# Kernel optimization log

Measured on AMD Instinct MI355X. Metric: run time of the kernel, lower is better.

Reference implementation:

```python
import jax, jax.numpy as jnp
import numpy as np

D_IN = 2048
D_OUT = 2048
H = 16
QK_ROPE = 64
QK_NOPE = 64
QK_HEAD = QK_NOPE + QK_ROPE  # 128
V_HEAD = 128
KV_RANK = 512
THETA = 10000.0
EPS = 1e-6


def rms_norm(x, w):
    var = jnp.mean(x * x, axis=-1, keepdims=True)
    return x * jax.lax.rsqrt(var + EPS) * w


def apply_rope(x, theta=THETA):
    # x: [B, S, H, D] with D even; interleaved-pair rotation (torchtune style)
    B, S, NH, D = x.shape
    half = D // 2
    freqs = 1.0 / (theta ** (jnp.arange(0, D, 2, dtype=jnp.float32) / D))  # [D/2]
    ang = jnp.arange(S, dtype=jnp.float32)[:, None] * freqs[None, :]       # [S, D/2]
    cos = jnp.cos(ang)[None, :, None, :]  # [1,S,1,D/2]
    sin = jnp.sin(ang)[None, :, None, :]
    xp = x.reshape(B, S, NH, half, 2)
    x1, x2 = xp[..., 0], xp[..., 1]
    out = jnp.stack([x1 * cos - x2 * sin, x2 * cos + x1 * sin], axis=-1)
    return out.reshape(B, S, NH, D).astype(x.dtype)


def setup_inputs() -> dict:
    key = jax.random.key(0)
    ks = jax.random.split(key, 6)
    B, S = 2, 2048
    s = lambda fan_in: 1.0 / np.sqrt(fan_in)
    x = jax.random.normal(ks[0], (B, S, D_IN), dtype=jnp.float32)
    w_query = jax.random.uniform(ks[1], (D_IN, H * QK_HEAD), jnp.float32, -s(D_IN), s(D_IN))
    wkv_a = jax.random.uniform(ks[2], (D_IN, KV_RANK + QK_ROPE), jnp.float32, -s(D_IN), s(D_IN))
    wkv_b = jax.random.uniform(ks[3], (KV_RANK, H * (QK_NOPE + V_HEAD)), jnp.float32, -s(KV_RANK), s(KV_RANK))
    kv_norm_w = jnp.ones((KV_RANK,), jnp.float32)
    out_proj_w = jax.random.uniform(ks[4], (H * V_HEAD, D_OUT), jnp.float32, -s(H * V_HEAD), s(H * V_HEAD))
    return {"x": x, "w_query": w_query, "wkv_a": wkv_a, "wkv_b": wkv_b,
            "kv_norm_w": kv_norm_w, "out_proj_w": out_proj_w}


def reference(x, w_query, wkv_a, wkv_b, kv_norm_w, out_proj_w):
    B, S, _ = x.shape
    scale = QK_HEAD ** -0.5
    # queries (no q-lora)
    q = (x @ w_query).reshape(B, S, H, QK_HEAD)
    # low-rank KV compression
    kv = x @ wkv_a                                    # [B,S,KV_RANK+QK_ROPE]
    kv_c, k_pe = kv[..., :KV_RANK], kv[..., KV_RANK:]
    kv_dec = (rms_norm(kv_c, kv_norm_w) @ wkv_b).reshape(B, S, H, QK_NOPE + V_HEAD)
    k_nope, v = kv_dec[..., :QK_NOPE], kv_dec[..., QK_NOPE:]
    k_pe = jnp.broadcast_to(k_pe[:, :, None, :], (B, S, H, QK_ROPE))
    q_nope, q_pe = q[..., :QK_NOPE], q[..., QK_NOPE:]
    q_pe = apply_rope(q_pe)
    k_pe = apply_rope(k_pe)
    queries = jnp.concatenate([q_nope, q_pe], axis=-1)   # [B,S,H,QK_HEAD]
    keys = jnp.concatenate([k_nope, k_pe], axis=-1)
    # attention
    scores = jnp.einsum('bqhd,bkhd->bhqk', queries, keys) * scale
    mask = jnp.triu(jnp.ones((S, S), dtype=bool), k=1)
    scores = jnp.where(mask[None, None], -jnp.inf, scores)
    attn = jax.nn.softmax(scores.astype(jnp.float32), axis=-1).astype(x.dtype)
    out = jnp.einsum('bhqk,bkhd->bqhd', attn, v).reshape(B, S, H * V_HEAD)
    return out @ out_proj_w
```

## Files before the change

kernel.cpp:

```cpp
#include <hip/hip_runtime.h>
#include <hip/hip_bf16.h>
#include <math.h>

#define BATCH   2
#define SEQ     2048
#define D_IN    2048
#define NHEAD   16
#define QK_ROPE 64
#define QK_NOPE 64
#define QK_HEAD 128
#define V_HEAD  128
#define KV_RANK 512
#define KV_W    640
#define NTOK    (BATCH*SEQ)
#define EPS_F   1e-6f

typedef unsigned short u16;
typedef short bf16x8 __attribute__((ext_vector_type(8)));
typedef float f32x4  __attribute__((ext_vector_type(4)));

__device__ __forceinline__ u16 f2bf(float f) {
    unsigned u = __float_as_uint(f);
    return (u16)((u + 0x7fffu + ((u >> 16) & 1u)) >> 16);
}
__device__ __forceinline__ float bf2f(u16 u) {
    return __uint_as_float(((unsigned)u) << 16);
}
__device__ __forceinline__ float exp2_hw(float x) {
    float r;
    asm volatile("v_exp_f32 %0, %1\n\ts_nop 0" : "=v"(r) : "v"(x));
    return r;
}
__device__ __forceinline__ void gload16(const void* g, void* l) {
    __builtin_amdgcn_global_load_lds((const __attribute__((address_space(1))) unsigned int*)g,
                                     (__attribute__((address_space(3))) unsigned int*)l, 16, 0, 0);
}

__global__ __launch_bounds__(256) void convert_bf16(const float* __restrict__ src,
                                                    u16* __restrict__ dst, int n4) {
    int gid = blockIdx.x * 256 + threadIdx.x;
    if (gid >= n4) return;
    float4 v = ((const float4*)src)[gid];
    unsigned lo = (unsigned)f2bf(v.x) | ((unsigned)f2bf(v.y) << 16);
    unsigned hi = (unsigned)f2bf(v.z) | ((unsigned)f2bf(v.w) << 16);
    ((uint2*)dst)[gid] = make_uint2(lo, hi);
}

__global__ __launch_bounds__(256) void transpose_bf16(const float* __restrict__ src,
                                                      u16* __restrict__ dst,
                                                      int N, int K) {
    __shared__ float tile[32][33];
    const int nb = blockIdx.x * 32, kb = blockIdx.y * 32;
    const int tx = threadIdx.x, ty = threadIdx.y;
#pragma unroll
    for (int i = 0; i < 4; ++i) {
        int k = kb + ty + 8 * i, n = nb + tx;
        tile[ty + 8 * i][tx] = (n < N) ? src[(size_t)k * N + n] : 0.f;
    }
    __syncthreads();
#pragma unroll
    for (int i = 0; i < 4; ++i) {
        int n = nb + ty + 8 * i, k = kb + tx;
        dst[(size_t)n * K + k] = f2bf(tile[tx][ty + 8 * i]);
    }
}

__global__ __launch_bounds__(256) void rope_table_kernel(float* __restrict__ tab) {
    int gid = blockIdx.x * 256 + threadIdx.x;
    int i = gid & 31, s = gid >> 5;
    float freq = __expf(-(float)(2 * i) / 64.0f * 9.210340371976184f);
    float ang = (float)s * freq;
    tab[2 * gid]     = cosf(ang);
    tab[2 * gid + 1] = sinf(ang);
}

template <int EPI>
__global__ __launch_bounds__(512, 1) void gemm256(const u16* __restrict__ A,
                                                  const u16* __restrict__ BT,
                                                  void* __restrict__ out0,
                                                  void* __restrict__ out1,
                                                  const float* __restrict__ tab,
                                                  int gx, int N, int K, float oscale) {
    __shared__ u16 lds[65536];
    const int tid = threadIdx.x;
    const int w = tid >> 6, l = tid & 63;
    const int lr = l & 15, lg = l >> 4;
    const int wr = w >> 2;
    const int wc = w & 3;
    const int nwg = gridDim.x, q8 = nwg >> 3;
    const int wg = (blockIdx.x & 7) * q8 + (blockIdx.x >> 3);
    const int row0 = (wg / gx) * 256, col0 = (wg % gx) * 256;
    const int NT = K >> 6;

    f32x4 acc[8][4];
#pragma unroll
    for (int m = 0; m < 8; ++m)
#pragma unroll
        for (int n = 0; n < 4; ++n) acc[m][n] = (f32x4){0.f, 0.f, 0.f, 0.f};

    auto stageA = [&](int bufi, int h, int kt) {
        u16* base = lds + bufi * 16384 + h * 8192;
        const u16* g = A + (size_t)(row0 + h * 128) * K + kt * 64;
#pragma unroll
        for (int i = 0; i < 2; ++i) {
            int L = (i * 512 + tid) * 16;
            int s = L ^ (((L >> 7) & 7) << 4);
            gload16(g + (size_t)(s >> 7) * K + ((s & 127) >> 1), base + (L >> 1));
        }
    };
    auto stageB = [&](int bufi, int h, int kt) {
        u16* base = lds + 32768 + bufi * 16384 + h * 8192;
        const u16* g = BT + (size_t)(col0 + h * 128) * K + kt * 64;
#pragma unroll
        for (int i = 0; i < 2; ++i) {
            int L = (i * 512 + tid) * 16;
            int s = L ^ (((L >> 7) & 7) << 4);
            gload16(g + (size_t)(s >> 7) * K + ((s & 127) >> 1), base + (L >> 1));
        }
    };

    stageB(0, 0, 0); stageB(0, 1, 0); stageA(0, 0, 0); stageA(0, 1, 0);

    const int bhalf = wc >> 1;
    const int brow0 = (wc & 1) * 64;

    for (int t = 0; t < NT; ++t) {
        const int buf = t & 1, nb = buf ^ 1;
        u16* Ab = lds + buf * 16384 + wr * 8192;
        u16* Bb = lds + 32768 + buf * 16384 + bhalf * 8192;

#pragma unroll
        for (int q = 0; q < 4; ++q) {
            const int mh = q >> 1, ks = q & 1;
            if (q == 0) {
                asm volatile("s_waitcnt vmcnt(2)" ::: "memory");
                __builtin_amdgcn_s_barrier();
                __builtin_amdgcn_sched_barrier(0);
            } else if (q == 2) {
                if (t + 1 < NT) asm volatile("s_waitcnt vmcnt(4)" ::: "memory");
                else            asm volatile("s_waitcnt vmcnt(0)" ::: "memory");
                __builtin_amdgcn_s_barrier();
                __builtin_amdgcn_sched_barrier(0);
            }
            bf16x8 af[4], bfg[4];
#pragma unroll
            for (int i = 0; i < 4; ++i) {
                int row = (mh * 4 + i) * 16 + lr;
                int byte = row * 128 + ks * 64 + lg * 16;
                af[i] = *(const bf16x8*)&Ab[(byte ^ ((row & 7) << 4)) >> 1];
            }
#pragma unroll
            for (int n = 0; n < 4; ++n) {
                int row = brow0 + n * 16 + lr;
                int byte = row * 128 + ks * 64 + lg * 16;
                bfg[n] = *(const bf16x8*)&Bb[(byte ^ ((row & 7) << 4)) >> 1];
            }
            if (t + 1 < NT) {
                if (q == 0)      stageB(nb, 0, t + 1);
                else if (q == 1) stageB(nb, 1, t + 1);
                else if (q == 2) stageA(nb, 0, t + 1);
                else             stageA(nb, 1, t + 1);
            }
            __builtin_amdgcn_s_barrier();
            asm volatile("s_waitcnt lgkmcnt(0)" ::: "memory");
            __builtin_amdgcn_sched_barrier(0);
            __builtin_amdgcn_s_setprio(1);
#pragma unroll
            for (int i = 0; i < 4; ++i)
#pragma unroll
                for (int n = 0; n < 4; ++n)
                    acc[mh * 4 + i][n] = __builtin_amdgcn_mfma_f32_16x16x32_bf16(
                        af[i], bfg[n], acc[mh * 4 + i][n], 0, 0, 0);
            __builtin_amdgcn_s_setprio(0);
        }
    }

    if (EPI == 0) {
        u16* qp = (u16*)out0;
        float* kvp = (float*)out1;
        const bool pe = (wc & 1);
#pragma unroll
        for (int m = 0; m < 8; ++m)
#pragma unroll
            for (int n = 0; n < 4; ++n) {
                int c = col0 + wc * 64 + n * 16 + lr;
#pragma unroll
                for (int j = 0; j < 4; ++j) {
                    int r = row0 + wr * 128 + m * 16 + 4 * lg + j;
                    float v = acc[m][n][j];
                    if (c < 2048) {
                        v *= oscale;
                        if (pe) {
                            int s = r & (SEQ - 1);
                            int ip = (16 * n + lr) >> 1;
                            float2 cs = ((const float2*)tab)[s * 32 + ip];
                            float part = __shfl_xor(v, 1);
                            v = (lr & 1) ? (v * cs.x + part * cs.y)
                                         : (v * cs.x - part * cs.y);
                        }
                        qp[(size_t)r * 2048 + c] = f2bf(v);
                    } else if (c < 2688) {
                        kvp[(size_t)r * KV_W + (c - 2048)] = v;
                    }
                }
            }
    } else {
        u16* Kall = (u16*)out0;
        u16* Vt   = (u16*)out1;
#pragma unroll
        for (int m = 0; m < 8; ++m) {
            int r0 = row0 + wr * 128 + m * 16 + 4 * lg;
            int b  = r0 >> 11;
            int s0 = r0 & (SEQ - 1);
#pragma unroll
            for (int n = 0; n < 4; ++n) {
                int c = col0 + wc * 64 + n * 16 + lr;
                int h = (unsigned)c / 192u;
                int cr = c - h * 192;
                int bh = b * NHEAD + h;
                if (cr < 64) {
#pragma unroll
                    for (int j = 0; j < 4; ++j) {
                        int s = s0 + j;
                        Kall[((size_t)bh * SEQ + s) * 128 + (cr ^ ((s & 7) << 3))] = f2bf(acc[m][n][j]);
                    }
                } else {
                    int d = cr - 64;
                    union { u16 u[4]; uint2 v; } pk;
#pragma unroll
                    for (int j = 0; j < 4; ++j) pk.u[j] = f2bf(acc[m][n][j]);
                    size_t base = ((size_t)bh * 128 + d) * SEQ + (s0 & ~63);
                    *(uint2*)&Vt[base + ((s0 & 63) ^ ((d & 7) << 3))] = pk.v;
                }
            }
        }
    }
}

__global__ __launch_bounds__(512, 1) void gemm_out(const u16* __restrict__ A,
                                                   const u16* __restrict__ BT,
                                                   float* __restrict__ C,
                                                   int N, int K) {
    __shared__ u16 lds[73728];
    const int tid = threadIdx.x;
    const int w = tid >> 6, l = tid & 63;
    const int lr = l & 15, lg = l >> 4;
    const int wr = w >> 1, wc = w & 1;
    const int nwg = gridDim.x, q8 = nwg >> 3;
    const int wg = (blockIdx.x & 7) * q8 + (blockIdx.x >> 3);
    const int gx = N >> 7;
    const int row0 = (wg / gx) * 256, col0 = (wg % gx) * 128;
    const int NT = K >> 6;

    f32x4 acc[4][4];
#pragma unroll
    for (int m = 0; m < 4; ++m)
#pragma unroll
        for (int n = 0; n < 4; ++n) acc[m][n] = (f32x4){0.f, 0.f, 0.f, 0.f};

    auto stageA = [&](int bufi, int h, int kt) {
        u16* base = lds + bufi * 16384 + h * 8192;
        const u16* g = A + (size_t)(row0 + h * 128) * K + kt * 64;
#pragma unroll
        for (int i = 0; i < 2; ++i) {
            int L = (i * 512 + tid) * 16;
            int s = L ^ (((L >> 7) & 7) << 4);
            gload16(g + (size_t)(s >> 7) * K + ((s & 127) >> 1), base + (L >> 1));
        }
    };
    auto stageB = [&](int bufi, int kt) {
        u16* base = lds + 49152 + bufi * 8192;
        const u16* g = BT + (size_t)col0 * K + kt * 64;
#pragma unroll
        for (int i = 0; i < 2; ++i) {
            int L = (i * 512 + tid) * 16;
            int s = L ^ (((L >> 7) & 7) << 4);
            gload16(g + (size_t)(s >> 7) * K + ((s & 127) >> 1), base + (L >> 1));
        }
    };

    stageA(0, 0, 0); stageA(0, 1, 0); stageB(0, 0);
    stageA(1, 0, 1); stageA(1, 1, 1); stageB(1, 1);

    const int ar0 = (wr & 1) * 64;

    for (int t = 0; t < NT; ++t) {
        const int buf = t % 3, nb2 = (t + 2) % 3;
        u16* Ab = lds + buf * 16384 + (wr >> 1) * 8192;
        u16* Bb = lds + 49152 + buf * 8192;
        if (t + 1 < NT) asm volatile("s_waitcnt vmcnt(6)" ::: "memory");
        else            asm volatile("s_waitcnt vmcnt(0)" ::: "memory");
        __builtin_amdgcn_s_barrier();
        __builtin_amdgcn_sched_barrier(0);

#pragma unroll
        for (int q = 0; q < 2; ++q) {
            bf16x8 af[4], bfg[4];
#pragma unroll
            for (int i = 0; i < 4; ++i) {
                int row = ar0 + i * 16 + lr;
                int byte = row * 128 + q * 64 + lg * 16;
                af[i] = *(const bf16x8*)&Ab[(byte ^ ((row & 7) << 4)) >> 1];
            }
#pragma unroll
            for (int n = 0; n < 4; ++n) {
                int row = wc * 64 + n * 16 + lr;
                int byte = row * 128 + q * 64 + lg * 16;
                bfg[n] = *(const bf16x8*)&Bb[(byte ^ ((row & 7) << 4)) >> 1];
            }
            if (t + 2 < NT) {
                if (q == 0) { stageA(nb2, 0, t + 2); stageA(nb2, 1, t + 2); }
                else        { stageB(nb2, t + 2); }
            }
            __builtin_amdgcn_s_barrier();
            asm volatile("s_waitcnt lgkmcnt(0)" ::: "memory");
            __builtin_amdgcn_sched_barrier(0);
            __builtin_amdgcn_s_setprio(1);
#pragma unroll
            for (int i = 0; i < 4; ++i)
#pragma unroll
                for (int n = 0; n < 4; ++n)
                    acc[i][n] = __builtin_amdgcn_mfma_f32_16x16x32_bf16(
                        af[i], bfg[n], acc[i][n], 0, 0, 0);
            __builtin_amdgcn_s_setprio(0);
        }
    }

#pragma unroll
    for (int m = 0; m < 4; ++m)
#pragma unroll
        for (int n = 0; n < 4; ++n) {
            int c = col0 + wc * 64 + n * 16 + lr;
#pragma unroll
            for (int j = 0; j < 4; ++j) {
                int r = row0 + wr * 64 + m * 16 + 4 * lg + j;
                C[(size_t)r * N + c] = acc[m][n][j];
            }
        }
}

__global__ __launch_bounds__(256) void rmsnorm_bf(const float* __restrict__ kv,
                                                  const float* __restrict__ w,
                                                  u16* __restrict__ c_norm) {
    __shared__ float red[256];
    const int row = blockIdx.x, t = threadIdx.x;
    const float* src = kv + (size_t)row * KV_W;
    float v0 = src[t], v1 = src[t + 256];
    red[t] = v0 * v0 + v1 * v1;
    __syncthreads();
    for (int s = 128; s > 0; s >>= 1) {
        if (t < s) red[t] += red[t + s];
        __syncthreads();
    }
    const float inv = rsqrtf(red[0] / (float)KV_RANK + EPS_F);
    u16* dst = c_norm + (size_t)row * KV_RANK;
    dst[t]       = f2bf(v0 * inv * w[t]);
    dst[t + 256] = f2bf(v1 * inv * w[t + 256]);
}

__global__ __launch_bounds__(256) void build_kpe(const float* __restrict__ kv,
                                                 const float* __restrict__ tab,
                                                 u16* __restrict__ K_all) {
    const int gid = blockIdx.x * 256 + threadIdx.x;
    const int dq = gid & 15;
    const int s = (gid >> 4) & (SEQ - 1);
    const int b = gid >> 15;
    const float* src = kv + (size_t)(b * SEQ + s) * KV_W + KV_RANK + 4 * dq;
    float4 v = *(const float4*)src;
    const int i0 = 2 * dq;
    float2 cs0 = ((const float2*)tab)[s * 32 + i0];
    float2 cs1 = ((const float2*)tab)[s * 32 + i0 + 1];
    union { u16 u[4]; uint2 w; } pk;
    pk.u[0] = f2bf(v.x * cs0.x - v.y * cs0.y);
    pk.u[1] = f2bf(v.y * cs0.x + v.x * cs0.y);
    pk.u[2] = f2bf(v.z * cs1.x - v.w * cs1.y);
    pk.u[3] = f2bf(v.w * cs1.x + v.z * cs1.y);
    const int idx = (64 + 4 * dq) ^ ((s & 7) << 3);
#pragma unroll
    for (int h = 0; h < NHEAD; ++h) {
        int bh = b * NHEAD + h;
        *(uint2*)&K_all[((size_t)bh * SEQ + s) * 128 + idx] = pk.w;
    }
}

#define QTILE 64
#define KTILE 64

__global__ __launch_bounds__(256, 2) void attn_mfma(const u16* __restrict__ q_bf,
                                                    const u16* __restrict__ K_all,
                                                    const u16* __restrict__ Vt,
                                                    u16* __restrict__ attn_bf) {
    __shared__ u16 Kbuf[2][KTILE * 128];
    __shared__ u16 Vbuf[2][128 * KTILE];
    __shared__ u16 Plds[4][16 * KTILE];

    const int idx = blockIdx.x;
    const int bh = (idx & 7) + 8 * (idx >> 7);
    const int pi = (idx >> 3) & 15;
    const int b = bh >> 4, h = bh & 15;

    const int tid = threadIdx.x;
    const int w = tid >> 6, l = tid & 63;
    const int lr = l & 15, lg = l >> 4;
    const u16* Kb = K_all + (size_t)bh * SEQ * 128;
    const u16* Vb = Vt + (size_t)bh * 128 * SEQ;
    const int sw = (lr & 7) << 3;
    u16* pw = Plds[w];

    auto stage = [&](int bufi, int k0) {
        u16* kb = Kbuf[bufi];
        u16* vb = Vbuf[bufi];
#pragma unroll
        for (int it = 0; it < 4; ++it) {
            int ci = it * 256 + tid;
            gload16(Kb + (((size_t)(k0 + (ci >> 4))) << 7) + ((ci & 15) << 3),
                    kb + (ci << 3));
        }
#pragma unroll
        for (int it = 0; it < 4; ++it) {
            int ci = it * 256 + tid;
            gload16(Vb + (size_t)(ci >> 3) * SEQ + k0 + ((ci & 7) << 3),
                    vb + (ci << 3));
        }
    };

    const int qbA = (31 - pi) * QTILE;
    const int qbB = pi * QTILE;

    stage(0, 0);
    int cur = 0;
    for (int half = 0; half < 2; ++half) {
        const int qbase = half ? qbB : qbA;
        const int nkt = (qbase >> 6) + 1;
        const int qg = qbase + 16 * w + lr;

        const u16* qrow = q_bf + (size_t)(b * SEQ + qg) * 2048 + h * QK_HEAD;
        bf16x8 qf[4];
#pragma unroll
        for (int dc = 0; dc < 4; ++dc) qf[dc] = *(const bf16x8*)(qrow + dc * 32 + lg * 8);

        f32x4 oacc[8];
#pragma unroll
        for (int ft = 0; ft < 8; ++ft) oacc[ft] = (f32x4){0.f, 0.f, 0.f, 0.f};
        float m_r = -1e30f, l_r = 0.f;

        for (int kt = 0; kt < nkt; ++kt) {
            const int k0 = kt * KTILE;
            if (kt + 1 < nkt) {
                stage(cur ^ 1, k0 + KTILE);
                asm volatile("s_waitcnt vmcnt(8)" ::: "memory");
            } else if (half == 0) {
                stage(cur ^ 1, 0);
                asm volatile("s_waitcnt vmcnt(8)" ::: "memory");
            } else {
                asm volatile("s_waitcnt vmcnt(0)" ::: "memory");
            }
            __builtin_amdgcn_s_barrier();
            __builtin_amdgcn_sched_barrier(0);

            const u16* kb = Kbuf[cur];
            const u16* vb = Vbuf[cur];

            f32x4 s[4];
            __builtin_amdgcn_s_setprio(1);
#pragma unroll
            for (int f = 0; f < 4; ++f) {
                s[f] = (f32x4){0.f, 0.f, 0.f, 0.f};
#pragma unroll
                for (int dc = 0; dc < 4; ++dc) {
                    bf16x8 kf = *(const bf16x8*)&kb[(16 * f + lr) * 128 + ((32 * dc + 8 * lg) ^ sw)];
                    s[f] = __builtin_amdgcn_mfma_f32_16x16x32_bf16(kf, qf[dc], s[f], 0, 0, 0);
                }
            }
            __builtin_amdgcn_s_setprio(0);

            if (kt == nkt - 1) {
#pragma unroll
                for (int f = 0; f < 4; ++f)
#pragma unroll
                    for (int j = 0; j < 4; ++j)
                        if (k0 + 16 * f + 4 * lg + j > qg) s[f][j] = -1e30f;
            }

            float t0 = fmaxf(fmaxf(s[0][0], s[0][1]), fmaxf(s[0][2], s[0][3]));
            float t1 = fmaxf(fmaxf(s[1][0], s[1][1]), fmaxf(s[1][2], s[1][3]));
            float t2 = fmaxf(fmaxf(s[2][0], s[2][1]), fmaxf(s[2][2], s[2][3]));
            float t3 = fmaxf(fmaxf(s[3][0], s[3][1]), fmaxf(s[3][2], s[3][3]));
            float t = fmaxf(fmaxf(t0, t1), fmaxf(t2, t3));
            t = fmaxf(t, __shfl_xor(t, 16));
            t = fmaxf(t, __shfl_xor(t, 32));
            bool up = (t > m_r + 11.5f);
            float newm = up ? t : m_r;
            float sf_ = up ? exp2_hw(m_r - t) : 1.0f;
            m_r = newm;
            float rs = 0.f;
#pragma unroll
            for (int f = 0; f < 4; ++f)
#pragma unroll
                for (int j = 0; j < 4; ++j) {
                    float p = exp2_hw(s[f][j] - newm);
                    s[f][j] = p;
                    rs += p;
                }
            rs += __shfl_xor(rs, 16);
            rs += __shfl_xor(rs, 32);
            l_r = l_r * sf_ + rs;
            if (__any(up)) {
#pragma unroll
                for (int ft = 0; ft < 8; ++ft)
#pragma unroll
                    for (int j = 0; j < 4; ++j) oacc[ft][j] *= sf_;
            }

#pragma unroll
            for (int f = 0; f < 4; ++f) {
                union { u16 u[4]; uint2 v; } pk;
#pragma unroll
                for (int j = 0; j < 4; ++j) pk.u[j] = f2bf(s[f][j]);
                *(uint2*)&pw[lr * 64 + ((16 * f + 4 * lg) ^ sw)] = pk.v;
            }
            asm volatile("s_waitcnt lgkmcnt(0)" ::: "memory");
            bf16x8 pfr[2];
#pragma unroll
            for (int ks = 0; ks < 2; ++ks)
                pfr[ks] = *(const bf16x8*)&pw[lr * 64 + ((32 * ks + 8 * lg) ^ sw)];

            __builtin_amdgcn_s_setprio(1);
#pragma unroll
            for (int ft = 0; ft < 8; ++ft) {
                int d = 16 * ft + lr;
#pragma unroll
                for (int ks = 0; ks < 2; ++ks) {
                    bf16x8 vf = *(const bf16x8*)&vb[d * 64 + ((32 * ks + 8 * lg) ^ sw)];
                    oacc[ft] = __builtin_amdgcn_mfma_f32_16x16x32_bf16(vf, pfr[ks], oacc[ft], 0, 0, 0);
                }
            }
            __builtin_amdgcn_s_setprio(0);

            __builtin_amdgcn_s_barrier();
            cur ^= 1;
        }

        const float inv = 1.0f / l_r;
        u16* orow = attn_bf + (size_t)(b * SEQ + qg) * 2048 + h * V_HEAD;
#pragma unroll
        for (int ft = 0; ft < 8; ++ft) {
            union { u16 u[4]; uint2 v; } ok;
#pragma unroll
            for (int j = 0; j < 4; ++j) ok.u[j] = f2bf(oacc[ft][j] * inv);
            *(uint2*)(orow + 16 * ft + 4 * lg) = ok.v;
        }
    }
}

extern "C" void kernel_launch(void* const* d_in, const int* in_sizes, int n_in,
                              void* d_out, int out_size, void* d_ws, size_t ws_size,
                              hipStream_t stream) {
    const float* x         = (const float*)d_in[0];
    const float* w_query   = (const float*)d_in[1];
    const float* wkv_a     = (const float*)d_in[2];
    const float* wkv_b     = (const float*)d_in[3];
    const float* kv_norm_w = (const float*)d_in[4];
    const float* out_proj  = (const float*)d_in[5];

    u16* x_bf     = (u16*)d_ws;
    u16* q_bf     = x_bf + (size_t)8388608;
    u16* c_norm   = q_bf + (size_t)8388608;
    u16* kvdec_bf = c_norm + (size_t)2097152;
    u16* K_all    = kvdec_bf + (size_t)12582912;
    u16* Vt       = K_all + (size_t)8388608;
    u16* wT       = Vt + (size_t)8388608;
    u16* wkvaT    = wT + (size_t)4194304;
    u16* wkvbT    = wkvaT + (size_t)1310720;
    u16* opT      = wkvbT + (size_t)1572864;
    float* kv     = (float*)(opT + (size_t)4194304);
    float* tab    = kv + (size_t)2621440;
    u16* attn_bf  = x_bf;
    float* out = (float*)d_out;

    dim3 tb(32, 8);
    const float qscale2 = 0.08838834764831845f * 1.4426950408889634f;

    convert_bf16<<<8192, 256, 0, stream>>>(x, x_bf, 2097152);
    transpose_bf16<<<dim3(64, 64), tb, 0, stream>>>(w_query, wT, 2048, 2048);
    transpose_bf16<<<dim3(20, 64), tb, 0, stream>>>(wkv_a, wkvaT, 576, 2048);
    transpose_bf16<<<dim3(96, 16), tb, 0, stream>>>(wkv_b, wkvbT, 3072, 512);
    transpose_bf16<<<dim3(64, 64), tb, 0, stream>>>(out_proj, opT, 2048, 2048);
    rope_table_kernel<<<256, 256, 0, stream>>>(tab);

    gemm256<0><<<176, 512, 0, stream>>>(x_bf, wT, q_bf, kv, tab,
                                        11, 2688, 2048, qscale2);
    rmsnorm_bf<<<NTOK, 256, 0, stream>>>(kv, kv_norm_w, c_norm);
    gemm256<2><<<192, 512, 0, stream>>>(c_norm, wkvbT, K_all, Vt, nullptr,
                                        12, 3072, 512, 1.0f);
    build_kpe<<<256, 256, 0, stream>>>(kv, tab, K_all);

    attn_mfma<<<512, 256, 0, stream>>>(q_bf, K_all, Vt, attn_bf);

    gemm_out<<<256, 512, 0, stream>>>(attn_bf, opT, out, 2048, 2048);
}
```

Baseline: 250.4 us.

## Triple-buffer GEMM with K-tile 32, merge prep kernels, fuse k_pe rope into rmsnorm

The shared 256x256 GEMM now stages 32-wide K tiles into a three-slot LDS ring, prefetching two tiles ahead with a narrower 4-way swizzle, instead of double-buffered 64-wide tiles. This aims to hide global-load latency better and shrink LDS use, at the cost of twice as many barrier-synchronised iterations. The input conversion, four weight transposes and the rope table are merged into one block-range-dispatched prep kernel to cut launch overhead. The k_pe rope and broadcast into K_all is folded into the rmsnorm kernel, removing the separate build_kpe launch and a reread of kv.

```diff
diff --git a/kernel.cpp b/kernel.cpp
--- a/kernel.cpp
+++ b/kernel.cpp
@@ -36,22 +36,12 @@
                                      (__attribute__((address_space(3))) unsigned int*)l, 16, 0, 0);
 }
 
-__global__ __launch_bounds__(256) void convert_bf16(const float* __restrict__ src,
-                                                    u16* __restrict__ dst, int n4) {
-    int gid = blockIdx.x * 256 + threadIdx.x;
-    if (gid >= n4) return;
-    float4 v = ((const float4*)src)[gid];
-    unsigned lo = (unsigned)f2bf(v.x) | ((unsigned)f2bf(v.y) << 16);
-    unsigned hi = (unsigned)f2bf(v.z) | ((unsigned)f2bf(v.w) << 16);
-    ((uint2*)dst)[gid] = make_uint2(lo, hi);
-}
-
-__global__ __launch_bounds__(256) void transpose_bf16(const float* __restrict__ src,
-                                                      u16* __restrict__ dst,
-                                                      int N, int K) {
-    __shared__ float tile[32][33];
-    const int nb = blockIdx.x * 32, kb = blockIdx.y * 32;
-    const int tx = threadIdx.x, ty = threadIdx.y;
+__device__ __forceinline__ void transpose_sec(const float* __restrict__ src,
+                                              u16* __restrict__ dst,
+                                              int N, int K, int bx, int by,
+                                              float (*tile)[33], int tid) {
+    const int tx = tid & 31, ty = tid >> 5;
+    const int nb = bx * 32, kb = by * 32;
 #pragma unroll
     for (int i = 0; i < 4; ++i) {
         int k = kb + ty + 8 * i, n = nb + tx;
@@ -65,13 +55,41 @@
     }
 }
 
-__global__ __launch_bounds__(256) void rope_table_kernel(float* __restrict__ tab) {
-    int gid = blockIdx.x * 256 + threadIdx.x;
-    int i = gid & 31, s = gid >> 5;
-    float freq = __expf(-(float)(2 * i) / 64.0f * 9.210340371976184f);
-    float ang = (float)s * freq;
-    tab[2 * gid]     = cosf(ang);
-    tab[2 * gid + 1] = sinf(ang);
+__global__ __launch_bounds__(256) void prep(const float* __restrict__ x, u16* __restrict__ x_bf,
+                                            const float* __restrict__ wq, u16* __restrict__ wqT,
+                                            const float* __restrict__ wkva, u16* __restrict__ wkvaT,
+                                            const float* __restrict__ wkvb, u16* __restrict__ wkvbT,
+                                            const float* __restrict__ op, u16* __restrict__ opT,
+                                            float* __restrict__ tab) {
+    __shared__ float tile[32][33];
+    const int idx = blockIdx.x;
+    const int tid = threadIdx.x;
+    if (idx < 8192) {
+        int gid = idx * 256 + tid;
+        float4 v = ((const float4*)x)[gid];
+        unsigned lo = (unsigned)f2bf(v.x) | ((unsigned)f2bf(v.y) << 16);
+        unsigned hi = (unsigned)f2bf(v.z) | ((unsigned)f2bf(v.w) << 16);
+        ((uint2*)x_bf)[gid] = make_uint2(lo, hi);
+    } else if (idx < 12288) {
+        int s = idx - 8192;
+        transpose_sec(wq, wqT, 2048, 2048, s % 64, s / 64, tile, tid);
+    } else if (idx < 13568) {
+        int s = idx - 12288;
+        transpose_sec(wkva, wkvaT, 576, 2048, s % 20, s / 20, tile, tid);
+    } else if (idx < 15104) {
+        int s = idx - 13568;
+        transpose_sec(wkvb, wkvbT, 3072, 512, s % 96, s / 96, tile, tid);
+    } else if (idx < 19200) {
+        int s = idx - 15104;
+        transpose_sec(op, opT, 2048, 2048, s % 64, s / 64, tile, tid);
+    } else {
+        int gid = (idx - 19200) * 256 + tid;
+        int i = gid & 31, s = gid >> 5;
+        float freq = __expf(-(float)(2 * i) / 64.0f * 9.210340371976184f);
+        float ang = (float)s * freq;
+        tab[2 * gid]     = cosf(ang);
+        tab[2 * gid + 1] = sinf(ang);
+    }
 }
 
 template <int EPI>
@@ -81,7 +99,7 @@
                                                   void* __restrict__ out1,
                                                   const float* __restrict__ tab,
                                                   int gx, int N, int K, float oscale) {
-    __shared__ u16 lds[65536];
+    __shared__ u16 lds[49152];
     const int tid = threadIdx.x;
     const int w = tid >> 6, l = tid & 63;
     const int lr = l & 15, lg = l >> 4;
@@ -90,7 +108,7 @@
     const int nwg = gridDim.x, q8 = nwg >> 3;
     const int wg = (blockIdx.x & 7) * q8 + (blockIdx.x >> 3);
     const int row0 = (wg / gx) * 256, col0 = (wg % gx) * 256;
-    const int NT = K >> 6;
+    const int NT = K >> 5;
 
     f32x4 acc[8][4];
 #pragma unroll
@@ -98,81 +116,77 @@
 #pragma unroll
         for (int n = 0; n < 4; ++n) acc[m][n] = (f32x4){0.f, 0.f, 0.f, 0.f};
 
-    auto stageA = [&](int bufi, int h, int kt) {
-        u16* base = lds + bufi * 16384 + h * 8192;
-        const u16* g = A + (size_t)(row0 + h * 128) * K + kt * 64;
+    auto stageA = [&](int bufi, int kt) {
+        u16* base = lds + bufi * 8192;
+        const u16* g = A + (size_t)row0 * K + kt * 32;
 #pragma unroll
         for (int i = 0; i < 2; ++i) {
             int L = (i * 512 + tid) * 16;
-            int s = L ^ (((L >> 7) & 7) << 4);
-            gload16(g + (size_t)(s >> 7) * K + ((s & 127) >> 1), base + (L >> 1));
+            int s = L ^ (((L >> 6) & 3) << 4);
+            gload16(g + (size_t)(L >> 6) * K + ((s & 63) >> 1), base + (L >> 1));
         }
     };
-    auto stageB = [&](int bufi, int h, int kt) {
-        u16* base = lds + 32768 + bufi * 16384 + h * 8192;
-        const u16* g = BT + (size_t)(col0 + h * 128) * K + kt * 64;
+    auto stageB = [&](int bufi, int kt) {
+        u16* base = lds + 24576 + bufi * 8192;
+        const u16* g = BT + (size_t)col0 * K + kt * 32;
 #pragma unroll
         for (int i = 0; i < 2; ++i) {
             int L = (i * 512 + tid) * 16;
-            int s = L ^ (((L >> 7) & 7) << 4);
-            gload16(g + (size_t)(s >> 7) * K + ((s & 127) >> 1), base + (L >> 1));
+            int s = L ^ (((L >> 6) & 3) << 4);
+            gload16(g + (size_t)(L >> 6) * K + ((s & 63) >> 1), base + (L >> 1));
         }
     };
 
-    stageB(0, 0, 0); stageB(0, 1, 0); stageA(0, 0, 0); stageA(0, 1, 0);
-
-    const int bhalf = wc >> 1;
-    const int brow0 = (wc & 1) * 64;
+    stageA(0, 0); stageB(0, 0); stageA(1, 1); stageB(1, 1);
 
     for (int t = 0; t < NT; ++t) {
-        const int buf = t & 1, nb = buf ^ 1;
-        u16* Ab = lds + buf * 16384 + wr * 8192;
-        u16* Bb = lds + 32768 + buf * 16384 + bhalf * 8192;
-
-#pragma unroll
-        for (int q = 0; q < 4; ++q) {
-            const int mh = q >> 1, ks = q & 1;
-            if (q == 0) {
-                asm volatile("s_waitcnt vmcnt(2)" ::: "memory");
-                __builtin_amdgcn_s_barrier();
-                __builtin_amdgcn_sched_barrier(0);
-            } else if (q == 2) {
-                if (t + 1 < NT) asm volatile("s_waitcnt vmcnt(4)" ::: "memory");
-                else            asm volatile("s_waitcnt vmcnt(0)" ::: "memory");
-                __builtin_amdgcn_s_barrier();
-                __builtin_amdgcn_sched_barrier(0);
-            }
-            bf16x8 af[4], bfg[4];
-#pragma unroll
-            for (int i = 0; i < 4; ++i) {
-                int row = (mh * 4 + i) * 16 + lr;
-                int byte = row * 128 + ks * 64 + lg * 16;
-                af[i] = *(const bf16x8*)&Ab[(byte ^ ((row & 7) << 4)) >> 1];
-            }
-#pragma unroll
-            for (int n = 0; n < 4; ++n) {
-                int row = brow0 + n * 16 + lr;
-                int byte = row * 128 + ks * 64 + lg * 16;
-                bfg[n] = *(const bf16x8*)&Bb[(byte ^ ((row & 7) << 4)) >> 1];
-            }
-            if (t + 1 < NT) {
-                if (q == 0)      stageB(nb, 0, t + 1);
-                else if (q == 1) stageB(nb, 1, t + 1);
-                else if (q == 2) stageA(nb, 0, t + 1);
-                else             stageA(nb, 1, t + 1);
-            }
-            __builtin_amdgcn_s_barrier();
-            asm volatile("s_waitcnt lgkmcnt(0)" ::: "memory");
-            __builtin_amdgcn_sched_barrier(0);
-            __builtin_amdgcn_s_setprio(1);
-#pragma unroll
-            for (int i = 0; i < 4; ++i)
-#pragma unroll
-                for (int n = 0; n < 4; ++n)
-                    acc[mh * 4 + i][n] = __builtin_amdgcn_mfma_f32_16x16x32_bf16(
-                        af[i], bfg[n], acc[mh * 4 + i][n], 0, 0, 0);
-            __builtin_amdgcn_s_setprio(0);
-        }
+        const int buf = t % 3, nb2 = (t + 2) % 3;
+        u16* Ab = lds + buf * 8192;
+        u16* Bb = lds + 24576 + buf * 8192;
+        if (t + 1 < NT) asm volatile("s_waitcnt vmcnt(4)" ::: "memory");
+        else            asm volatile("s_waitcnt vmcnt(0)" ::: "memory");
+        __builtin_amdgcn_s_barrier();
+        __builtin_amdgcn_sched_barrier(0);
+
+        bf16x8 bfg[4], af[4];
+#pragma unroll
+        for (int n = 0; n < 4; ++n) {
+            int row = wc * 64 + n * 16 + lr;
+            bfg[n] = *(const bf16x8*)&Bb[row * 32 + (((lg * 16) ^ ((row & 3) << 4)) >> 1)];
+        }
+#pragma unroll
+        for (int i = 0; i < 4; ++i) {
+            int row = wr * 128 + i * 16 + lr;
+            af[i] = *(const bf16x8*)&Ab[row * 32 + (((lg * 16) ^ ((row & 3) << 4)) >> 1)];
+        }
+        if (t + 2 < NT) stageA(nb2, t + 2);
+        __builtin_amdgcn_s_barrier();
+        asm volatile("s_waitcnt lgkmcnt(0)" ::: "memory");
+        __builtin_amdgcn_sched_barrier(0);
+        __builtin_amdgcn_s_setprio(1);
+#pragma unroll
+        for (int i = 0; i < 4; ++i)
+#pragma unroll
+            for (int n = 0; n < 4; ++n)
+                acc[i][n] = __builtin_amdgcn_mfma_f32_16x16x32_bf16(af[i], bfg[n], acc[i][n], 0, 0, 0);
+        __builtin_amdgcn_s_setprio(0);
+
+#pragma unroll
+        for (int i = 0; i < 4; ++i) {
+            int row = wr * 128 + (4 + i) * 16 + lr;
+            af[i] = *(const bf16x8*)&Ab[row * 32 + (((lg * 16) ^ ((row & 3) << 4)) >> 1)];
+        }
+        if (t + 2 < NT) stageB(nb2, t + 2);
+        __builtin_amdgcn_s_barrier();
+        asm volatile("s_waitcnt lgkmcnt(0)" ::: "memory");
+        __builtin_amdgcn_sched_barrier(0);
+        __builtin_amdgcn_s_setprio(1);
+#pragma unroll
+        for (int i = 0; i < 4; ++i)
+#pragma unroll
+            for (int n = 0; n < 4; ++n)
+                acc[4 + i][n] = __builtin_amdgcn_mfma_f32_16x16x32_bf16(af[i], bfg[n], acc[4 + i][n], 0, 0, 0);
+        __builtin_amdgcn_s_setprio(0);
     }
 
     if (EPI == 0) {
@@ -341,7 +355,9 @@
 
 __global__ __launch_bounds__(256) void rmsnorm_bf(const float* __restrict__ kv,
                                                   const float* __restrict__ w,
-                                                  u16* __restrict__ c_norm) {
+                                                  u16* __restrict__ c_norm,
+                                                  const float* __restrict__ tab,
+                                                  u16* __restrict__ K_all) {
     __shared__ float red[256];
     const int row = blockIdx.x, t = threadIdx.x;
     const float* src = kv + (size_t)row * KV_W;
@@ -356,30 +372,26 @@
     u16* dst = c_norm + (size_t)row * KV_RANK;
     dst[t]       = f2bf(v0 * inv * w[t]);
     dst[t + 256] = f2bf(v1 * inv * w[t + 256]);
-}
-
-__global__ __launch_bounds__(256) void build_kpe(const float* __restrict__ kv,
-                                                 const float* __restrict__ tab,
-                                                 u16* __restrict__ K_all) {
-    const int gid = blockIdx.x * 256 + threadIdx.x;
-    const int dq = gid & 15;
-    const int s = (gid >> 4) & (SEQ - 1);
-    const int b = gid >> 15;
-    const float* src = kv + (size_t)(b * SEQ + s) * KV_W + KV_RANK + 4 * dq;
-    float4 v = *(const float4*)src;
-    const int i0 = 2 * dq;
-    float2 cs0 = ((const float2*)tab)[s * 32 + i0];
-    float2 cs1 = ((const float2*)tab)[s * 32 + i0 + 1];
-    union { u16 u[4]; uint2 w; } pk;
-    pk.u[0] = f2bf(v.x * cs0.x - v.y * cs0.y);
-    pk.u[1] = f2bf(v.y * cs0.x + v.x * cs0.y);
-    pk.u[2] = f2bf(v.z * cs1.x - v.w * cs1.y);
-    pk.u[3] = f2bf(v.w * cs1.x + v.z * cs1.y);
-    const int idx = (64 + 4 * dq) ^ ((s & 7) << 3);
-#pragma unroll
-    for (int h = 0; h < NHEAD; ++h) {
-        int bh = b * NHEAD + h;
-        *(uint2*)&K_all[((size_t)bh * SEQ + s) * 128 + idx] = pk.w;
+
+    if (t < 16) {
+        const int dq = t;
+        const int s = row & (SEQ - 1);
+        const int b = row >> 11;
+        float4 v = *(const float4*)(src + KV_RANK + 4 * dq);
+        const int i0 = 2 * dq;
+        float2 cs0 = ((const float2*)tab)[s * 32 + i0];
+        float2 cs1 = ((const float2*)tab)[s * 32 + i0 + 1];
+        union { u16 u[4]; uint2 w2; } pk;
+        pk.u[0] = f2bf(v.x * cs0.x - v.y * cs0.y);
+        pk.u[1] = f2bf(v.y * cs0.x + v.x * cs0.y);
+        pk.u[2] = f2bf(v.z * cs1.x - v.w * cs1.y);
+        pk.u[3] = f2bf(v.w * cs1.x + v.z * cs1.y);
+        const int idx = (64 + 4 * dq) ^ ((s & 7) << 3);
+#pragma unroll
+        for (int h = 0; h < NHEAD; ++h) {
+            int bh = b * NHEAD + h;
+            *(uint2*)&K_all[((size_t)bh * SEQ + s) * 128 + idx] = pk.w2;
+        }
     }
 }
 
@@ -578,22 +590,16 @@
     u16* attn_bf  = x_bf;
     float* out = (float*)d_out;
 
-    dim3 tb(32, 8);
     const float qscale2 = 0.08838834764831845f * 1.4426950408889634f;
 
-    convert_bf16<<<8192, 256, 0, stream>>>(x, x_bf, 2097152);
-    transpose_bf16<<<dim3(64, 64), tb, 0, stream>>>(w_query, wT, 2048, 2048);
-    transpose_bf16<<<dim3(20, 64), tb, 0, stream>>>(wkv_a, wkvaT, 576, 2048);
-    transpose_bf16<<<dim3(96, 16), tb, 0, stream>>>(wkv_b, wkvbT, 3072, 512);
-    transpose_bf16<<<dim3(64, 64), tb, 0, stream>>>(out_proj, opT, 2048, 2048);
-    rope_table_kernel<<<256, 256, 0, stream>>>(tab);
+    prep<<<19456, 256, 0, stream>>>(x, x_bf, w_query, wT, wkv_a, wkvaT,
+                                    wkv_b, wkvbT, out_proj, opT, tab);
 
     gemm256<0><<<176, 512, 0, stream>>>(x_bf, wT, q_bf, kv, tab,
                                         11, 2688, 2048, qscale2);
-    rmsnorm_bf<<<NTOK, 256, 0, stream>>>(kv, kv_norm_w, c_norm);
+    rmsnorm_bf<<<NTOK, 256, 0, stream>>>(kv, kv_norm_w, c_norm, tab, K_all);
     gemm256<2><<<192, 512, 0, stream>>>(c_norm, wkvbT, K_all, Vt, nullptr,
                                         12, 3072, 512, 1.0f);
-    build_kpe<<<256, 256, 0, stream>>>(kv, tab, K_all);
 
     attn_mfma<<<512, 256, 0, stream>>>(q_bf, K_all, Vt, attn_bf);
 
```

After: 246.5 us. Within noise of the previous version (-1.5%).
